# Performance work log

Measured on AMD Instinct MI355X. Metric: run time of the kernel, lower is better.

## Reference

```python
import jax, jax.numpy as jnp
import numpy as np

B, S, E, H = 8, 2048, 1024, 64

def setup_inputs() -> dict:
    key = jax.random.key(0)
    k1, k2, k3, k4 = jax.random.split(key, 4)
    scale = 0.02
    return {
        "x": jax.random.normal(k1, (B, S, E), dtype=jnp.float32),
        "Wq": jax.random.normal(k2, (E, H), dtype=jnp.float32) * scale,
        "Wk": jax.random.normal(k3, (E, H), dtype=jnp.float32) * scale,
        "Wv": jax.random.normal(k4, (E, H), dtype=jnp.float32) * scale,
    }

def reference(x, Wq, Wk, Wv):
    # x: [B, S, E]; projections to [B, S, H]
    q = jnp.einsum("bse,eh->bsh", x, Wq)
    k = jnp.einsum("bse,eh->bsh", x, Wk)
    v = jnp.einsum("bse,eh->bsh", x, Wv)
    head_size = Wq.shape[1]
    # NOTE: original divides by head_size (not sqrt(head_size))
    scores = jnp.einsum("bqh,bkh->bqk", q, k) / head_size  # [B, S, S]
    seq = q.shape[1]
    causal = jnp.tril(jnp.ones((seq, seq), dtype=bool))
    scores = jnp.where(causal, scores, -jnp.inf)
    attn = jax.nn.softmax(scores, axis=-1)
    # dropout p=0.0 (eval) -> identity
    return jnp.einsum("bqk,bkh->bqh", attn, v)
```

## Files before the change

### kernel.cpp

```cpp
#include <hip/hip_runtime.h>


typedef __bf16 bf16;
typedef bf16 bf16x8 __attribute__((ext_vector_type(8)));
typedef bf16 bf16x4 __attribute__((ext_vector_type(4)));
typedef float v4f __attribute__((ext_vector_type(4)));

#define MFMA_BF16 __builtin_amdgcn_mfma_f32_16x16x32_bf16

constexpr int SEQ = 2048, EDIM = 1024, HDIM = 64;
constexpr float SCALE_L2E = 1.4426950408889634f / 64.0f;

#define AS1 __attribute__((address_space(1)))
#define AS3 __attribute__((address_space(3)))
static __device__ __forceinline__ void gload_lds16(const void* g, void* l) {
  __builtin_amdgcn_global_load_lds((const AS1 unsigned int*)g,
                                   (AS3 unsigned int*)l, 16, 0, 0);
}

__global__ __launch_bounds__(256) void prep_w_kernel(
    const float* __restrict__ Wq, const float* __restrict__ Wk,
    const float* __restrict__ Wv, bf16* __restrict__ Wt) {
  int mat = blockIdx.x >> 5, kseg = blockIdx.x & 31;
  const float* src = mat == 0 ? Wq : (mat == 1 ? Wk : Wv);
  int n = threadIdx.x & 63;
  int k0 = kseg * 32 + (threadIdx.x >> 6) * 8;
  bf16x8 v;
#pragma unroll
  for (int j = 0; j < 8; ++j)
    v[j] = (bf16)src[(k0 + j) * 64 + n];
  *reinterpret_cast<bf16x8*>(Wt + (size_t)(mat * 64 + n) * EDIM + k0) = v;
}

__global__ __launch_bounds__(256, 3) void proj_kernel(
    const float* __restrict__ x, const bf16* __restrict__ Wt,
    bf16* __restrict__ qw, bf16* __restrict__ kw, bf16* __restrict__ vT) {
  __shared__ __align__(16) bf16 Bs[2][192][64];

  const int t = threadIdx.x;
  const int m0 = blockIdx.x * 32;
  const int wv = t >> 6, lane = t & 63, quad = lane >> 4, l16 = lane & 15;

  v4f acc[2][3] = {};
  float4 aA[8], aB[8];

  auto loadA = [&](int kk, float4* dst) {
#pragma unroll
    for (int mi = 0; mi < 2; ++mi)
#pragma unroll
      for (int ks = 0; ks < 2; ++ks) {
        const float* p = x + (size_t)(m0 + 16 * mi + l16) * EDIM + kk * 64 +
                         32 * ks + 8 * quad;
        dst[(mi * 2 + ks) * 2 + 0] = *reinterpret_cast<const float4*>(p);
        dst[(mi * 2 + ks) * 2 + 1] = *reinterpret_cast<const float4*>(p + 4);
      }
  };
  auto issueB = [&](int kk, int buf) {
#pragma unroll
    for (int p = 0; p < 6; ++p) {
      int q = p * 64 + lane;
      int r = 48 * wv + (q >> 3), s = q & 7;
      const bf16* src = Wt + (size_t)r * EDIM + kk * 64 + (s ^ (r & 7)) * 8;
      bf16* dst = &Bs[buf][48 * wv + 8 * p][0];
      gload_lds16(src, dst);
    }
  };

  auto step = [&](int kk, int buf, const float4* aCur, float4* aNext) {
    if (kk < 15) {
      __builtin_amdgcn_sched_barrier(0);
      issueB(kk + 1, buf ^ 1);
      loadA(kk + 1, aNext);
      __builtin_amdgcn_sched_barrier(0);
      asm volatile("s_waitcnt vmcnt(14)" ::: "memory");
      __builtin_amdgcn_sched_barrier(0);
    } else {
      asm volatile("s_waitcnt vmcnt(0)" ::: "memory");
      __builtin_amdgcn_sched_barrier(0);
    }
    bf16x8 af[2][2];
#pragma unroll
    for (int mi = 0; mi < 2; ++mi)
#pragma unroll
      for (int ks = 0; ks < 2; ++ks) {
        const float4 f0 = aCur[(mi * 2 + ks) * 2 + 0];
        const float4 f1 = aCur[(mi * 2 + ks) * 2 + 1];
        af[mi][ks] = bf16x8{(bf16)f0.x, (bf16)f0.y, (bf16)f0.z, (bf16)f0.w,
                            (bf16)f1.x, (bf16)f1.y, (bf16)f1.z, (bf16)f1.w};
      }
    const char* bsb = (const char*)&Bs[buf][0][0];
#pragma unroll
    for (int ks = 0; ks < 2; ++ks) {
      bf16x8 bfr[3];
#pragma unroll
      for (int ni = 0; ni < 3; ++ni) {
        int R = 48 * wv + 16 * ni + l16;
        int off = (ks * 64 + quad * 16) ^ ((R & 7) << 4);
        bfr[ni] = *reinterpret_cast<const bf16x8*>(bsb + R * 128 + off);
      }
#pragma unroll
      for (int mi = 0; mi < 2; ++mi)
#pragma unroll
        for (int ni = 0; ni < 3; ++ni)
          acc[mi][ni] = MFMA_BF16(af[mi][ks], bfr[ni], acc[mi][ni], 0, 0, 0);
    }
  };

  loadA(0, aA);
  issueB(0, 0);
#pragma unroll 1
  for (int k2 = 0; k2 < 8; ++k2) {
    step(2 * k2 + 0, 0, aA, aB);
    step(2 * k2 + 1, 1, aB, aA);
  }

#pragma unroll
  for (int mi = 0; mi < 2; ++mi) {
    const int token0 = m0 + 16 * mi + 4 * quad;
#pragma unroll
    for (int ni = 0; ni < 3; ++ni) {
      int n = 48 * wv + 16 * ni + l16;
      if (n < 64) {
#pragma unroll
        for (int r = 0; r < 4; ++r)
          qw[(size_t)(token0 + r) * HDIM + n] = (bf16)acc[mi][ni][r];
      } else if (n < 128) {
#pragma unroll
        for (int r = 0; r < 4; ++r)
          kw[(size_t)(token0 + r) * HDIM + (n - 64)] = (bf16)acc[mi][ni][r];
      } else {
        int b = token0 >> 11, s0 = token0 & 2047;
        bf16x4 pk = {(bf16)acc[mi][ni][0], (bf16)acc[mi][ni][1],
                     (bf16)acc[mi][ni][2], (bf16)acc[mi][ni][3]};
        *reinterpret_cast<bf16x4*>(
            vT + ((size_t)(b * 64 + (n - 128))) * SEQ + s0) = pk;
      }
    }
  }
}

__global__ __launch_bounds__(512) void attn_kernel(
    const bf16* __restrict__ qw, const bf16* __restrict__ kw,
    const bf16* __restrict__ vT, float* __restrict__ out) {
  const int batch = blockIdx.x & 7;
  const int pi = blockIdx.x >> 3;
  const int w = threadIdx.x >> 6;
  const int lane = threadIdx.x & 63;
  const int quad = lane >> 4, l16 = lane & 15;

  __shared__ __align__(16) bf16 p_lds[8][2][32][68];
  __shared__ __align__(16) float o_lds[8][32][68];
  __shared__ float l_lds[8][32];

  const bf16* qB = qw + (size_t)batch * SEQ * HDIM;
  const bf16* kB = kw + (size_t)batch * SEQ * HDIM;
  const bf16* vB = vT + (size_t)batch * HDIM * SEQ;

  for (int sp = 0; sp < 2; ++sp) {
    const int j = sp ? (63 - pi) : pi;
    const int q0 = 32 * j;
    const int T64 = (j + 2) >> 1;
    const int nw = (T64 > w) ? (((T64 - 1 - w) >> 3) + 1) : 0;

    bf16x8 aq[2][2];
#pragma unroll
    for (int mi = 0; mi < 2; ++mi)
#pragma unroll
      for (int kf = 0; kf < 2; ++kf)
        aq[mi][kf] = *reinterpret_cast<const bf16x8*>(
            qB + (size_t)(q0 + 16 * mi + l16) * HDIM + 32 * kf + 8 * quad);

    v4f accO[2][4] = {};
    float l_part[2][4] = {{0.f, 0.f, 0.f, 0.f}, {0.f, 0.f, 0.f, 0.f}};
    bf16x8 kfr[4][2];

    auto loadK = [&](int jt) {
#pragma unroll
      for (int nt = 0; nt < 4; ++nt)
#pragma unroll
        for (int kf = 0; kf < 2; ++kf)
          kfr[nt][kf] = *reinterpret_cast<const bf16x8*>(
              kB + (size_t)(64 * jt + 16 * nt + l16) * HDIM + 32 * kf +
              8 * quad);
    };
    auto qk_exp_stage = [&](int jt, int slot) {
      v4f s[2][4] = {};
#pragma unroll
      for (int mi = 0; mi < 2; ++mi)
#pragma unroll
        for (int nt = 0; nt < 4; ++nt) {
          s[mi][nt] = MFMA_BF16(aq[mi][0], kfr[nt][0], s[mi][nt], 0, 0, 0);
          s[mi][nt] = MFMA_BF16(aq[mi][1], kfr[nt][1], s[mi][nt], 0, 0, 0);
        }
      const bool last = (jt == T64 - 1);
#pragma unroll
      for (int mi = 0; mi < 2; ++mi)
#pragma unroll
        for (int nt = 0; nt < 4; ++nt)
#pragma unroll
          for (int r = 0; r < 4; ++r) {
            float p = __builtin_amdgcn_exp2f(s[mi][nt][r] * SCALE_L2E);
            if (last &&
                (64 * jt + 16 * nt + l16 > q0 + 16 * mi + 4 * quad + r))
              p = 0.f;
            l_part[mi][r] += p;
            p_lds[w][slot][16 * mi + 4 * quad + r][16 * nt + l16] = (bf16)p;
          }
    };

    if (nw > 0) {
      loadK(w);
      qk_exp_stage(w, 0);
    }
    for (int i = 0; i < nw; ++i) {
      const int jt = w + 8 * i;
      const int k0 = 64 * jt;
      if (i + 1 < nw) loadK(jt + 8);
      bf16x8 vfr[4][2];
#pragma unroll
      for (int nt = 0; nt < 4; ++nt)
#pragma unroll
        for (int kc = 0; kc < 2; ++kc)
          vfr[nt][kc] = *reinterpret_cast<const bf16x8*>(
              vB + (size_t)(16 * nt + l16) * SEQ + k0 + 32 * kc + 8 * quad);
      asm volatile("s_waitcnt lgkmcnt(0)" ::: "memory");
      bf16x8 pa[2][2];
#pragma unroll
      for (int mi = 0; mi < 2; ++mi)
#pragma unroll
        for (int kc = 0; kc < 2; ++kc)
          pa[mi][kc] = *reinterpret_cast<const bf16x8*>(
              &p_lds[w][i & 1][16 * mi + l16][32 * kc + 8 * quad]);
      if (i + 1 < nw) qk_exp_stage(jt + 8, (i + 1) & 1);
#pragma unroll
      for (int mi = 0; mi < 2; ++mi)
#pragma unroll
        for (int nt = 0; nt < 4; ++nt) {
          accO[mi][nt] = MFMA_BF16(pa[mi][0], vfr[nt][0], accO[mi][nt], 0, 0, 0);
          accO[mi][nt] = MFMA_BF16(pa[mi][1], vfr[nt][1], accO[mi][nt], 0, 0, 0);
        }
    }

#pragma unroll
    for (int mi = 0; mi < 2; ++mi)
#pragma unroll
      for (int r = 0; r < 4; ++r) {
        float s = l_part[mi][r];
        s += __shfl_xor(s, 1, 16);
        s += __shfl_xor(s, 2, 16);
        s += __shfl_xor(s, 4, 16);
        s += __shfl_xor(s, 8, 16);
        l_part[mi][r] = s;
      }

    __syncthreads();
#pragma unroll
    for (int mi = 0; mi < 2; ++mi)
#pragma unroll
      for (int nt = 0; nt < 4; ++nt)
#pragma unroll
        for (int r = 0; r < 4; ++r)
          o_lds[w][16 * mi + 4 * quad + r][16 * nt + l16] = accO[mi][nt][r];
    if (l16 == 0) {
#pragma unroll
      for (int mi = 0; mi < 2; ++mi)
#pragma unroll
        for (int r = 0; r < 4; ++r)
          l_lds[w][16 * mi + 4 * quad + r] = l_part[mi][r];
    }
    __syncthreads();

    {
      const int col = threadIdx.x & 63;
      const int r0 = (threadIdx.x >> 6) * 4;
#pragma unroll
      for (int k = 0; k < 4; ++k) {
        const int row = r0 + k;
        float lt = 0.f, s = 0.f;
#pragma unroll
        for (int c = 0; c < 8; ++c) {
          lt += l_lds[c][row];
          s += o_lds[c][row][col];
        }
        out[((size_t)batch * SEQ + q0 + row) * HDIM + col] = s / lt;
      }
    }
  }
}

extern "C" void kernel_launch(void* const* d_in, const int* in_sizes, int n_in,
                              void* d_out, int out_size, void* d_ws,
                              size_t ws_size, hipStream_t stream) {
  const float* x = (const float*)d_in[0];
  const float* Wq = (const float*)d_in[1];
  const float* Wk = (const float*)d_in[2];
  const float* Wv = (const float*)d_in[3];

  char* ws = (char*)d_ws;
  bf16* Wt = (bf16*)(ws);
  bf16* qw = (bf16*)(ws + 0x60000);
  bf16* kw = (bf16*)(ws + 0x260000);
  bf16* vT = (bf16*)(ws + 0x460000);

  prep_w_kernel<<<96, 256, 0, stream>>>(Wq, Wk, Wv, Wt);
  proj_kernel<<<512, 256, 0, stream>>>(x, Wt, qw, kw, vT);
  attn_kernel<<<256, 512, 0, stream>>>(qw, kw, vT, (float*)d_out);
}
```

Measured before the change: 151.5 us.

## Share x tile across waves via LDS instead of per-wave redundant loads

Previously every wave loaded the full 32x64 fp32 x slice into registers, so each element was fetched and converted to bf16 four times per block. Now each thread loads 8 floats once, converts them and writes a swizzled bf16 tile into LDS that all waves read as MFMA A-fragments. This cuts redundant global loads and register pressure. In exchange it adds two extra barriers per k-step and a single-buffered A tile, which serialises more of the pipeline.

```diff
diff --git a/kernel.cpp b/kernel.cpp
--- a/kernel.cpp
+++ b/kernel.cpp
@@ -36,24 +36,27 @@
     const float* __restrict__ x, const bf16* __restrict__ Wt,
     bf16* __restrict__ qw, bf16* __restrict__ kw, bf16* __restrict__ vT) {
   __shared__ __align__(16) bf16 Bs[2][192][64];
+  __shared__ __align__(16) bf16 Ash[32][64];
 
   const int t = threadIdx.x;
   const int m0 = blockIdx.x * 32;
   const int wv = t >> 6, lane = t & 63, quad = lane >> 4, l16 = lane & 15;
+  const int arow = t >> 3;
+  const int aslot = t & 7;
 
   v4f acc[2][3] = {};
-  float4 aA[8], aB[8];
-
-  auto loadA = [&](int kk, float4* dst) {
-#pragma unroll
-    for (int mi = 0; mi < 2; ++mi)
-#pragma unroll
-      for (int ks = 0; ks < 2; ++ks) {
-        const float* p = x + (size_t)(m0 + 16 * mi + l16) * EDIM + kk * 64 +
-                         32 * ks + 8 * quad;
-        dst[(mi * 2 + ks) * 2 + 0] = *reinterpret_cast<const float4*>(p);
-        dst[(mi * 2 + ks) * 2 + 1] = *reinterpret_cast<const float4*>(p + 4);
-      }
+  float4 aR0, aR1;
+
+  auto loadA = [&](int kk) {
+    const float* p = x + (size_t)(m0 + arow) * EDIM + kk * 64 + aslot * 8;
+    aR0 = *reinterpret_cast<const float4*>(p);
+    aR1 = *reinterpret_cast<const float4*>(p + 4);
+  };
+  auto writeA = [&]() {
+    bf16x8 h = {(bf16)aR0.x, (bf16)aR0.y, (bf16)aR0.z, (bf16)aR0.w,
+                (bf16)aR1.x, (bf16)aR1.y, (bf16)aR1.z, (bf16)aR1.w};
+    *reinterpret_cast<bf16x8*>((char*)&Ash[0][0] + arow * 128 +
+                               ((aslot ^ (arow & 7)) * 16)) = h;
   };
   auto issueB = [&](int kk, int buf) {
 #pragma unroll
@@ -66,29 +69,37 @@
     }
   };
 
-  auto step = [&](int kk, int buf, const float4* aCur, float4* aNext) {
+  loadA(0);
+  issueB(0, 0);
+  asm volatile("s_waitcnt vmcnt(6)" ::: "memory");
+  __builtin_amdgcn_sched_barrier(0);
+  writeA();
+  asm volatile("s_waitcnt lgkmcnt(0)" ::: "memory");
+  __builtin_amdgcn_s_barrier();
+
+#pragma unroll 1
+  for (int kk = 0; kk < 16; ++kk) {
+    const int buf = kk & 1;
     if (kk < 15) {
-      __builtin_amdgcn_sched_barrier(0);
+      loadA(kk + 1);
       issueB(kk + 1, buf ^ 1);
-      loadA(kk + 1, aNext);
-      __builtin_amdgcn_sched_barrier(0);
-      asm volatile("s_waitcnt vmcnt(14)" ::: "memory");
-      __builtin_amdgcn_sched_barrier(0);
+      asm volatile("s_waitcnt vmcnt(8)" ::: "memory");
     } else {
       asm volatile("s_waitcnt vmcnt(0)" ::: "memory");
-      __builtin_amdgcn_sched_barrier(0);
-    }
+    }
+    __builtin_amdgcn_sched_barrier(0);
+
+    const char* asb = (const char*)&Ash[0][0];
+    const char* bsb = (const char*)&Bs[buf][0][0];
     bf16x8 af[2][2];
 #pragma unroll
     for (int mi = 0; mi < 2; ++mi)
 #pragma unroll
       for (int ks = 0; ks < 2; ++ks) {
-        const float4 f0 = aCur[(mi * 2 + ks) * 2 + 0];
-        const float4 f1 = aCur[(mi * 2 + ks) * 2 + 1];
-        af[mi][ks] = bf16x8{(bf16)f0.x, (bf16)f0.y, (bf16)f0.z, (bf16)f0.w,
-                            (bf16)f1.x, (bf16)f1.y, (bf16)f1.z, (bf16)f1.w};
-      }
-    const char* bsb = (const char*)&Bs[buf][0][0];
+        int row = 16 * mi + l16;
+        int off = ((4 * ks + quad) ^ (row & 7)) * 16;
+        af[mi][ks] = *reinterpret_cast<const bf16x8*>(asb + row * 128 + off);
+      }
 #pragma unroll
     for (int ks = 0; ks < 2; ++ks) {
       bf16x8 bfr[3];
@@ -104,14 +115,18 @@
         for (int ni = 0; ni < 3; ++ni)
           acc[mi][ni] = MFMA_BF16(af[mi][ks], bfr[ni], acc[mi][ni], 0, 0, 0);
     }
-  };
-
-  loadA(0, aA);
-  issueB(0, 0);
-#pragma unroll 1
-  for (int k2 = 0; k2 < 8; ++k2) {
-    step(2 * k2 + 0, 0, aA, aB);
-    step(2 * k2 + 1, 1, aB, aA);
+
+    if (kk < 15) {
+      asm volatile("s_waitcnt lgkmcnt(0)" ::: "memory");
+      __builtin_amdgcn_sched_barrier(0);
+      __builtin_amdgcn_s_barrier();
+      asm volatile("s_waitcnt vmcnt(6)" ::: "memory");
+      __builtin_amdgcn_sched_barrier(0);
+      writeA();
+      asm volatile("s_waitcnt lgkmcnt(0)" ::: "memory");
+      __builtin_amdgcn_sched_barrier(0);
+      __builtin_amdgcn_s_barrier();
+    }
   }
 
 #pragma unroll
```

After: 138.3 us. 8.7% less time.
